# Kernel optimization log

Hardware: AMD Instinct MI355X
Metric: run time of the kernel (lower is better)

## Reference

```python
import jax, jax.numpy as jnp
import numpy as np

NUM_CLASSES = 1000
FEAT_DIM = 256
BATCH = 8192
MARGIN = 5.0
ALPHA = 1.0
BETA = 1.0


def setup_inputs() -> dict:
    key = jax.random.key(0)
    k1, k2, k3 = jax.random.split(key, 3)
    x = jax.random.normal(k1, (BATCH, FEAT_DIM), dtype=jnp.float32)
    labels = jax.random.randint(k2, (BATCH,), 0, NUM_CLASSES, dtype=jnp.int64)
    centers = jax.random.normal(k3, (NUM_CLASSES, FEAT_DIM), dtype=jnp.float32)
    return {"x": x, "labels": labels, "centers": centers}


def reference(x, labels, centers):
    # --- intra-class part ---
    # distmat_intra[i, j] = ||x_i||^2 + ||x_j||^2 - 2 x_i . x_j  (then relu + sqrt)
    mag = jnp.sum(x * x, axis=1)                      # (B,)
    sim = x @ x.T                                     # (B, B)
    d2 = mag[None, :] + mag[:, None] - 2.0 * sim      # (B, B)
    d = jnp.sqrt(jax.nn.relu(d2))                     # (B, B)

    # mask[i, j] = labels[i] == labels[j]; original gathers masked values per row,
    # clamps to [1e-12, 1e12], sorts descending and uses only the top-2 values.
    mask = labels[:, None] == labels[None, :]         # (B, B) bool
    vals = jnp.where(mask, jnp.clip(d, 1e-12, 1e12), -jnp.inf)
    top2, _ = jax.lax.top_k(vals.reshape(-1), 2)      # two largest intra-class dists
    k = 2.0
    loss_intra = k / (1.0 / top2[0] + 1.0 / top2[1])  # harmonic mean * k

    # --- inter-class part (faithful to original broadcasting) ---
    # distmat_inter[i, j] = 2 ||c_j||^2 - 2 c_i . c_j
    cmag = 2.0 * jnp.sum(centers * centers, axis=1)   # (C,)
    inter = cmag[None, :] - 2.0 * (centers @ centers.T)
    inter = jnp.clip(inter.reshape(-1), 1e-12, 1e12)
    loss_inter = jnp.clip(MARGIN - jnp.min(inter), 0.0, 1e6)

    return ALPHA * loss_intra + BETA * loss_inter
```

## Files before the change

### kernel.cpp

```cpp
#include <hip/hip_runtime.h>
#include <math.h>

#define BATCH 8192
#define FEAT  256
#define NCLS  1000

#define NGEMM   528
#define NINTRA  NCLS
#define ROWCAP  24
#define MEMCAP  96


__global__ __launch_bounds__(512) void k_intra(const float* __restrict__ x,
                                               const int* __restrict__ labels,
                                               float* __restrict__ ws) {
    __shared__ __align__(16) float rowS[ROWCAP][256];
    __shared__ int   mem[MEMCAP];
    __shared__ float magS[MEMCAP];
    __shared__ float wred[8];
    __shared__ int cnt;
    int t = threadIdx.x;
    int lane = t & 63, w = t >> 6;
    int c = blockIdx.x;

    if (t == 0) cnt = 0;
    __syncthreads();
    const int4* gl4 = reinterpret_cast<const int4*>(labels);
    #pragma unroll
    for (int k = 0; k < 4; ++k) {
        int idx = t + (k << 9);
        int4 lv = gl4[idx];
        int base = idx << 2;
        if (lv.x == c) { int p = atomicAdd(&cnt, 1); if (p < MEMCAP) mem[p] = base;     }
        if (lv.y == c) { int p = atomicAdd(&cnt, 1); if (p < MEMCAP) mem[p] = base + 1; }
        if (lv.z == c) { int p = atomicAdd(&cnt, 1); if (p < MEMCAP) mem[p] = base + 2; }
        if (lv.w == c) { int p = atomicAdd(&cnt, 1); if (p < MEMCAP) mem[p] = base + 3; }
    }
    __syncthreads();
    int n = cnt < MEMCAP ? cnt : MEMCAP;
    float vmax = 0.0f;
    if (n >= 2) {
        const float4* x4 = reinterpret_cast<const float4*>(x);
        for (int m = w; m < n; m += 8) {
            float4 v = x4[(size_t)mem[m] * 64 + lane];
            if (m < ROWCAP)
                *reinterpret_cast<float4*>(&rowS[m][lane << 2]) = v;
            float s = v.x * v.x + v.y * v.y + v.z * v.z + v.w * v.w;
            #pragma unroll
            for (int o = 32; o > 0; o >>= 1) s += __shfl_xor(s, o);
            if (lane == 0) magS[m] = s;
        }
        __syncthreads();
        int npairs = n * (n - 1) / 2;
        for (int p = w; p < npairs; p += 16) {
            int p2 = p + 8;
            bool has2 = (p2 < npairs);
            int a1 = 0, r1 = p;
            while (r1 >= n - 1 - a1) { r1 -= n - 1 - a1; ++a1; }
            int b1 = a1 + 1 + r1;
            int a2 = a1, b2 = b1;
            if (has2) {
                int r2 = p2; a2 = 0;
                while (r2 >= n - 1 - a2) { r2 -= n - 1 - a2; ++a2; }
                b2 = a2 + 1 + r2;
            }
            float4 va1 = (a1 < ROWCAP) ? *reinterpret_cast<float4*>(&rowS[a1][lane << 2])
                                       : x4[(size_t)mem[a1] * 64 + lane];
            float4 vb1 = (b1 < ROWCAP) ? *reinterpret_cast<float4*>(&rowS[b1][lane << 2])
                                       : x4[(size_t)mem[b1] * 64 + lane];
            float4 va2 = (a2 < ROWCAP) ? *reinterpret_cast<float4*>(&rowS[a2][lane << 2])
                                       : x4[(size_t)mem[a2] * 64 + lane];
            float4 vb2 = (b2 < ROWCAP) ? *reinterpret_cast<float4*>(&rowS[b2][lane << 2])
                                       : x4[(size_t)mem[b2] * 64 + lane];
            float s1 = va1.x * vb1.x + va1.y * vb1.y + va1.z * vb1.z + va1.w * vb1.w;
            float s2 = va2.x * vb2.x + va2.y * vb2.y + va2.z * vb2.z + va2.w * vb2.w;
            #pragma unroll
            for (int o = 32; o > 0; o >>= 1) {
                s1 += __shfl_xor(s1, o);
                s2 += __shfl_xor(s2, o);
            }
            float d2a = magS[a1] + magS[b1] - 2.0f * s1;
            float da  = sqrtf(fmaxf(d2a, 0.0f));
            da = fminf(fmaxf(da, 1e-12f), 1e12f);
            vmax = fmaxf(vmax, da);
            if (has2) {
                float d2b = magS[a2] + magS[b2] - 2.0f * s2;
                float db  = sqrtf(fmaxf(d2b, 0.0f));
                db = fminf(fmaxf(db, 1e-12f), 1e12f);
                vmax = fmaxf(vmax, db);
            }
        }
    }
    if (lane == 0) wred[w] = vmax;
    __syncthreads();
    if (t == 0) {
        float m = 0.0f;
        #pragma unroll
        for (int q = 0; q < 8; ++q) m = fmaxf(m, wred[q]);
        ws[NGEMM + c] = m;
    }
}

__global__ __launch_bounds__(256) void k_inter(const float* __restrict__ centers,
                                               float* __restrict__ ws) {
    __shared__ float As[32][34];
    __shared__ float Bs[32][34];
    __shared__ float cmagI[32], cmagJ[32];
    __shared__ float wred[4];
    int t = threadIdx.x;
    int lane = t & 63, w = t >> 6;

    int bi = 0, rem = blockIdx.x;
    while (rem >= 32 - bi) { rem -= 32 - bi; ++bi; }
    int bj = bi + rem;
    int i0 = bi * 32, j0 = bj * 32;

    for (int q = w; q < 32; q += 4) {
        int gi = i0 + q, gj = j0 + q;
        float sI = 0.0f, sJ = 0.0f;
        if (gi < NCLS) {
            float4 v = reinterpret_cast<const float4*>(centers + (size_t)gi * FEAT)[lane];
            sI = v.x * v.x + v.y * v.y + v.z * v.z + v.w * v.w;
        }
        if (gj < NCLS) {
            float4 v = reinterpret_cast<const float4*>(centers + (size_t)gj * FEAT)[lane];
            sJ = v.x * v.x + v.y * v.y + v.z * v.z + v.w * v.w;
        }
        #pragma unroll
        for (int o = 32; o > 0; o >>= 1) {
            sI += __shfl_xor(sI, o);
            sJ += __shfl_xor(sJ, o);
        }
        if (lane == 0) { cmagI[q] = 2.0f * sI; cmagJ[q] = 2.0f * sJ; }
    }

    int tx = t & 15, ty = t >> 4;
    float acc[2][2] = {{0.f, 0.f}, {0.f, 0.f}};
    for (int kk = 0; kk < FEAT; kk += 32) {
        {
            int row = t >> 3, q = t & 7;
            int col = kk + q * 4;
            int gi = i0 + row, gj = j0 + row;
            float4 av = (gi < NCLS)
                ? *reinterpret_cast<const float4*>(centers + (size_t)gi * FEAT + col)
                : make_float4(0.f, 0.f, 0.f, 0.f);
            float4 bv = (gj < NCLS)
                ? *reinterpret_cast<const float4*>(centers + (size_t)gj * FEAT + col)
                : make_float4(0.f, 0.f, 0.f, 0.f);
            As[q * 4 + 0][row] = av.x; As[q * 4 + 1][row] = av.y;
            As[q * 4 + 2][row] = av.z; As[q * 4 + 3][row] = av.w;
            Bs[q * 4 + 0][row] = bv.x; Bs[q * 4 + 1][row] = bv.y;
            Bs[q * 4 + 2][row] = bv.z; Bs[q * 4 + 3][row] = bv.w;
        }
        __syncthreads();
        #pragma unroll
        for (int k = 0; k < 32; ++k) {
            float2 a2 = *reinterpret_cast<float2*>(&As[k][ty * 2]);
            float2 b2 = *reinterpret_cast<float2*>(&Bs[k][tx * 2]);
            acc[0][0] += a2.x * b2.x; acc[0][1] += a2.x * b2.y;
            acc[1][0] += a2.y * b2.x; acc[1][1] += a2.y * b2.y;
        }
        __syncthreads();
    }
    float lmin = 1e30f;
    #pragma unroll
    for (int jj = 0; jj < 2; ++jj) {
        int J = j0 + tx * 2 + jj;
        #pragma unroll
        for (int ii = 0; ii < 2; ++ii) {
            int I = i0 + ty * 2 + ii;
            if (I < NCLS && J < NCLS) {
                float v1 = cmagJ[tx * 2 + jj] - 2.0f * acc[ii][jj];
                v1 = fminf(fmaxf(v1, 1e-12f), 1e12f);
                float v2 = cmagI[ty * 2 + ii] - 2.0f * acc[ii][jj];
                v2 = fminf(fmaxf(v2, 1e-12f), 1e12f);
                lmin = fminf(lmin, fminf(v1, v2));
            }
        }
    }
    #pragma unroll
    for (int o = 32; o > 0; o >>= 1) lmin = fminf(lmin, __shfl_xor(lmin, o));
    if (lane == 0) wred[w] = lmin;
    __syncthreads();
    if (t == 0) {
        float m = fminf(fminf(wred[0], wred[1]), fminf(wred[2], wred[3]));
        ws[blockIdx.x] = m;
    }
}

__global__ __launch_bounds__(256) void k_final(const float* __restrict__ ws,
                                               float* __restrict__ out) {
    __shared__ float smx[4], smn[4];
    int t = threadIdx.x, lane = t & 63, w = t >> 6;
    float mn = 1e30f, mx = 0.0f;
    for (int i = t; i < NGEMM; i += 256)  mn = fminf(mn, ws[i]);
    for (int i = t; i < NINTRA; i += 256) mx = fmaxf(mx, ws[NGEMM + i]);
    #pragma unroll
    for (int o = 32; o > 0; o >>= 1) {
        mx = fmaxf(mx, __shfl_xor(mx, o));
        mn = fminf(mn, __shfl_xor(mn, o));
    }
    if (lane == 0) { smx[w] = mx; smn[w] = mn; }
    __syncthreads();
    if (t == 0) {
        mx = fmaxf(fmaxf(smx[0], smx[1]), fmaxf(smx[2], smx[3]));
        mn = fminf(fminf(smn[0], smn[1]), fminf(smn[2], smn[3]));
        float M = fmaxf(mx, 1e-12f);
        float r = 1.0f / M;
        float li2 = 2.0f / (r + r);
        float m = fminf(mn, 1e12f);
        float linter = fminf(fmaxf(5.0f - m, 0.0f), 1e6f);
        out[0] = li2 + linter;
    }
}

extern "C" void kernel_launch(void* const* d_in, const int* in_sizes, int n_in,
                              void* d_out, int out_size, void* d_ws, size_t ws_size,
                              hipStream_t stream) {
    const float* x       = (const float*)d_in[0];
    const int*   labels  = (const int*)d_in[1];
    const float* centers = (const float*)d_in[2];
    float*        ws     = (float*)d_ws;
    float*        out    = (float*)d_out;

    k_intra<<<NINTRA, 512, 0, stream>>>(x, labels, ws);
    k_inter<<<NGEMM, 256, 0, stream>>>(centers, ws);
    k_final<<<1, 256, 0, stream>>>(ws, out);
}
```

Measured before the change: 100.4 us.

## Bucket samples by label globally and fuse intra/inter passes into one launch

Each of the 1000 intra blocks used to scan all 8192 labels itself. A prep kernel now computes row norms and buckets sample indices per class with global atomics, after a memset of the counts. The intra pair work is split across 4 blocks per class and merged with the inter-center GEMM blocks into a single launch, which improves occupancy and overlap. In exchange it adds a memset and an extra launch, drops the shared-memory row cache in favour of global (L2) loads, and lowers the per-class member cap to 64.

```diff
diff --git a/kernel.cpp b/kernel.cpp
--- a/kernel.cpp
+++ b/kernel.cpp
@@ -5,104 +5,38 @@
 #define FEAT  256
 #define NCLS  1000
 
-#define NGEMM   528
-#define NINTRA  NCLS
-#define ROWCAP  24
-#define MEMCAP  96
-
-
-__global__ __launch_bounds__(512) void k_intra(const float* __restrict__ x,
-                                               const int* __restrict__ labels,
-                                               float* __restrict__ ws) {
-    __shared__ __align__(16) float rowS[ROWCAP][256];
-    __shared__ int   mem[MEMCAP];
-    __shared__ float magS[MEMCAP];
-    __shared__ float wred[8];
-    __shared__ int cnt;
-    int t = threadIdx.x;
-    int lane = t & 63, w = t >> 6;
-    int c = blockIdx.x;
-
-    if (t == 0) cnt = 0;
-    __syncthreads();
-    const int4* gl4 = reinterpret_cast<const int4*>(labels);
+#define NGEMM  528
+#define REPL   4
+#define NPAIRB (REPL*NCLS)
+#define NBLK   (NGEMM + NPAIRB)
+#define SLOTC  64
+
+
+__global__ __launch_bounds__(256) void k_prep(const float* __restrict__ x,
+                                              const int* __restrict__ labels,
+                                              int* __restrict__ counts,
+                                              int* __restrict__ mem,
+                                              float* __restrict__ mag) {
+    int gw   = (blockIdx.x * 256 + threadIdx.x) >> 6;
+    int lane = threadIdx.x & 63;
+    float4 v = reinterpret_cast<const float4*>(x)[(size_t)gw * 64 + lane];
+    float s = v.x * v.x + v.y * v.y + v.z * v.z + v.w * v.w;
     #pragma unroll
-    for (int k = 0; k < 4; ++k) {
-        int idx = t + (k << 9);
-        int4 lv = gl4[idx];
-        int base = idx << 2;
-        if (lv.x == c) { int p = atomicAdd(&cnt, 1); if (p < MEMCAP) mem[p] = base;     }
-        if (lv.y == c) { int p = atomicAdd(&cnt, 1); if (p < MEMCAP) mem[p] = base + 1; }
-        if (lv.z == c) { int p = atomicAdd(&cnt, 1); if (p < MEMCAP) mem[p] = base + 2; }
-        if (lv.w == c) { int p = atomicAdd(&cnt, 1); if (p < MEMCAP) mem[p] = base + 3; }
-    }
-    __syncthreads();
-    int n = cnt < MEMCAP ? cnt : MEMCAP;
-    float vmax = 0.0f;
-    if (n >= 2) {
-        const float4* x4 = reinterpret_cast<const float4*>(x);
-        for (int m = w; m < n; m += 8) {
-            float4 v = x4[(size_t)mem[m] * 64 + lane];
-            if (m < ROWCAP)
-                *reinterpret_cast<float4*>(&rowS[m][lane << 2]) = v;
-            float s = v.x * v.x + v.y * v.y + v.z * v.z + v.w * v.w;
-            #pragma unroll
-            for (int o = 32; o > 0; o >>= 1) s += __shfl_xor(s, o);
-            if (lane == 0) magS[m] = s;
-        }
-        __syncthreads();
-        int npairs = n * (n - 1) / 2;
-        for (int p = w; p < npairs; p += 16) {
-            int p2 = p + 8;
-            bool has2 = (p2 < npairs);
-            int a1 = 0, r1 = p;
-            while (r1 >= n - 1 - a1) { r1 -= n - 1 - a1; ++a1; }
-            int b1 = a1 + 1 + r1;
-            int a2 = a1, b2 = b1;
-            if (has2) {
-                int r2 = p2; a2 = 0;
-                while (r2 >= n - 1 - a2) { r2 -= n - 1 - a2; ++a2; }
-                b2 = a2 + 1 + r2;
-            }
-            float4 va1 = (a1 < ROWCAP) ? *reinterpret_cast<float4*>(&rowS[a1][lane << 2])
-                                       : x4[(size_t)mem[a1] * 64 + lane];
-            float4 vb1 = (b1 < ROWCAP) ? *reinterpret_cast<float4*>(&rowS[b1][lane << 2])
-                                       : x4[(size_t)mem[b1] * 64 + lane];
-            float4 va2 = (a2 < ROWCAP) ? *reinterpret_cast<float4*>(&rowS[a2][lane << 2])
-                                       : x4[(size_t)mem[a2] * 64 + lane];
-            float4 vb2 = (b2 < ROWCAP) ? *reinterpret_cast<float4*>(&rowS[b2][lane << 2])
-                                       : x4[(size_t)mem[b2] * 64 + lane];
-            float s1 = va1.x * vb1.x + va1.y * vb1.y + va1.z * vb1.z + va1.w * vb1.w;
-            float s2 = va2.x * vb2.x + va2.y * vb2.y + va2.z * vb2.z + va2.w * vb2.w;
-            #pragma unroll
-            for (int o = 32; o > 0; o >>= 1) {
-                s1 += __shfl_xor(s1, o);
-                s2 += __shfl_xor(s2, o);
-            }
-            float d2a = magS[a1] + magS[b1] - 2.0f * s1;
-            float da  = sqrtf(fmaxf(d2a, 0.0f));
-            da = fminf(fmaxf(da, 1e-12f), 1e12f);
-            vmax = fmaxf(vmax, da);
-            if (has2) {
-                float d2b = magS[a2] + magS[b2] - 2.0f * s2;
-                float db  = sqrtf(fmaxf(d2b, 0.0f));
-                db = fminf(fmaxf(db, 1e-12f), 1e12f);
-                vmax = fmaxf(vmax, db);
-            }
-        }
-    }
-    if (lane == 0) wred[w] = vmax;
-    __syncthreads();
-    if (t == 0) {
-        float m = 0.0f;
-        #pragma unroll
-        for (int q = 0; q < 8; ++q) m = fmaxf(m, wred[q]);
-        ws[NGEMM + c] = m;
-    }
-}
-
-__global__ __launch_bounds__(256) void k_inter(const float* __restrict__ centers,
-                                               float* __restrict__ ws) {
+    for (int o = 32; o > 0; o >>= 1) s += __shfl_xor(s, o);
+    if (lane == 0) {
+        mag[gw] = s;
+        int c = labels[gw];
+        int pos = atomicAdd(&counts[c], 1);
+        if (pos < SLOTC) mem[c * SLOTC + pos] = gw;
+    }
+}
+
+__global__ __launch_bounds__(256) void k_fused(const float* __restrict__ x,
+                                               const float* __restrict__ centers,
+                                               const int* __restrict__ counts,
+                                               const int* __restrict__ mem,
+                                               const float* __restrict__ mag,
+                                               float* __restrict__ part) {
     __shared__ float As[32][34];
     __shared__ float Bs[32][34];
     __shared__ float cmagI[32], cmagJ[32];
@@ -110,91 +44,145 @@
     int t = threadIdx.x;
     int lane = t & 63, w = t >> 6;
 
-    int bi = 0, rem = blockIdx.x;
-    while (rem >= 32 - bi) { rem -= 32 - bi; ++bi; }
-    int bj = bi + rem;
-    int i0 = bi * 32, j0 = bj * 32;
-
-    for (int q = w; q < 32; q += 4) {
-        int gi = i0 + q, gj = j0 + q;
-        float sI = 0.0f, sJ = 0.0f;
-        if (gi < NCLS) {
-            float4 v = reinterpret_cast<const float4*>(centers + (size_t)gi * FEAT)[lane];
-            sI = v.x * v.x + v.y * v.y + v.z * v.z + v.w * v.w;
-        }
-        if (gj < NCLS) {
-            float4 v = reinterpret_cast<const float4*>(centers + (size_t)gj * FEAT)[lane];
-            sJ = v.x * v.x + v.y * v.y + v.z * v.z + v.w * v.w;
-        }
+    if (blockIdx.x < NGEMM) {
+        int bi = 0, rem = blockIdx.x;
+        while (rem >= 32 - bi) { rem -= 32 - bi; ++bi; }
+        int bj = bi + rem;
+        int i0 = bi * 32, j0 = bj * 32;
+
+        for (int q = w; q < 32; q += 4) {
+            int gi = i0 + q, gj = j0 + q;
+            float sI = 0.0f, sJ = 0.0f;
+            if (gi < NCLS) {
+                float4 v = reinterpret_cast<const float4*>(centers + (size_t)gi * FEAT)[lane];
+                sI = v.x * v.x + v.y * v.y + v.z * v.z + v.w * v.w;
+            }
+            if (gj < NCLS) {
+                float4 v = reinterpret_cast<const float4*>(centers + (size_t)gj * FEAT)[lane];
+                sJ = v.x * v.x + v.y * v.y + v.z * v.z + v.w * v.w;
+            }
+            #pragma unroll
+            for (int o = 32; o > 0; o >>= 1) {
+                sI += __shfl_xor(sI, o);
+                sJ += __shfl_xor(sJ, o);
+            }
+            if (lane == 0) { cmagI[q] = 2.0f * sI; cmagJ[q] = 2.0f * sJ; }
+        }
+
+        int tx = t & 15, ty = t >> 4;
+        float acc[2][2] = {{0.f, 0.f}, {0.f, 0.f}};
+        for (int kk = 0; kk < FEAT; kk += 32) {
+            {
+                int row = t >> 3, q = t & 7;
+                int col = kk + q * 4;
+                int gi = i0 + row, gj = j0 + row;
+                float4 av = (gi < NCLS)
+                    ? *reinterpret_cast<const float4*>(centers + (size_t)gi * FEAT + col)
+                    : make_float4(0.f, 0.f, 0.f, 0.f);
+                float4 bv = (gj < NCLS)
+                    ? *reinterpret_cast<const float4*>(centers + (size_t)gj * FEAT + col)
+                    : make_float4(0.f, 0.f, 0.f, 0.f);
+                As[q * 4 + 0][row] = av.x; As[q * 4 + 1][row] = av.y;
+                As[q * 4 + 2][row] = av.z; As[q * 4 + 3][row] = av.w;
+                Bs[q * 4 + 0][row] = bv.x; Bs[q * 4 + 1][row] = bv.y;
+                Bs[q * 4 + 2][row] = bv.z; Bs[q * 4 + 3][row] = bv.w;
+            }
+            __syncthreads();
+            #pragma unroll
+            for (int k = 0; k < 32; ++k) {
+                float2 a2 = *reinterpret_cast<float2*>(&As[k][ty * 2]);
+                float2 b2 = *reinterpret_cast<float2*>(&Bs[k][tx * 2]);
+                acc[0][0] += a2.x * b2.x; acc[0][1] += a2.x * b2.y;
+                acc[1][0] += a2.y * b2.x; acc[1][1] += a2.y * b2.y;
+            }
+            __syncthreads();
+        }
+        float lmin = 1e30f;
         #pragma unroll
-        for (int o = 32; o > 0; o >>= 1) {
-            sI += __shfl_xor(sI, o);
-            sJ += __shfl_xor(sJ, o);
-        }
-        if (lane == 0) { cmagI[q] = 2.0f * sI; cmagJ[q] = 2.0f * sJ; }
-    }
-
-    int tx = t & 15, ty = t >> 4;
-    float acc[2][2] = {{0.f, 0.f}, {0.f, 0.f}};
-    for (int kk = 0; kk < FEAT; kk += 32) {
-        {
-            int row = t >> 3, q = t & 7;
-            int col = kk + q * 4;
-            int gi = i0 + row, gj = j0 + row;
-            float4 av = (gi < NCLS)
-                ? *reinterpret_cast<const float4*>(centers + (size_t)gi * FEAT + col)
-                : make_float4(0.f, 0.f, 0.f, 0.f);
-            float4 bv = (gj < NCLS)
-                ? *reinterpret_cast<const float4*>(centers + (size_t)gj * FEAT + col)
-                : make_float4(0.f, 0.f, 0.f, 0.f);
-            As[q * 4 + 0][row] = av.x; As[q * 4 + 1][row] = av.y;
-            As[q * 4 + 2][row] = av.z; As[q * 4 + 3][row] = av.w;
-            Bs[q * 4 + 0][row] = bv.x; Bs[q * 4 + 1][row] = bv.y;
-            Bs[q * 4 + 2][row] = bv.z; Bs[q * 4 + 3][row] = bv.w;
-        }
+        for (int jj = 0; jj < 2; ++jj) {
+            int J = j0 + tx * 2 + jj;
+            #pragma unroll
+            for (int ii = 0; ii < 2; ++ii) {
+                int I = i0 + ty * 2 + ii;
+                if (I < NCLS && J < NCLS) {
+                    float v1 = cmagJ[tx * 2 + jj] - 2.0f * acc[ii][jj];
+                    v1 = fminf(fmaxf(v1, 1e-12f), 1e12f);
+                    float v2 = cmagI[ty * 2 + ii] - 2.0f * acc[ii][jj];
+                    v2 = fminf(fmaxf(v2, 1e-12f), 1e12f);
+                    lmin = fminf(lmin, fminf(v1, v2));
+                }
+            }
+        }
+        #pragma unroll
+        for (int o = 32; o > 0; o >>= 1) lmin = fminf(lmin, __shfl_xor(lmin, o));
+        if (lane == 0) wred[w] = lmin;
         __syncthreads();
-        #pragma unroll
-        for (int k = 0; k < 32; ++k) {
-            float2 a2 = *reinterpret_cast<float2*>(&As[k][ty * 2]);
-            float2 b2 = *reinterpret_cast<float2*>(&Bs[k][tx * 2]);
-            acc[0][0] += a2.x * b2.x; acc[0][1] += a2.x * b2.y;
-            acc[1][0] += a2.y * b2.x; acc[1][1] += a2.y * b2.y;
-        }
+        if (t == 0) {
+            float m = fminf(fminf(wred[0], wred[1]), fminf(wred[2], wred[3]));
+            part[blockIdx.x] = m;
+        }
+    } else {
+        int bidp = blockIdx.x - NGEMM;
+        int c = bidp >> 2, r = bidp & 3;
+        int n = counts[c]; if (n > SLOTC) n = SLOTC;
+        float vmax = 0.0f;
+        if (n >= 2) {
+            const float4* x4 = reinterpret_cast<const float4*>(x);
+            const int* memc = mem + c * SLOTC;
+            int npairs = n * (n - 1) / 2;
+            for (int p = r * 4 + w; p < npairs; p += 32) {
+                int p2 = p + 16;
+                bool has2 = (p2 < npairs);
+                int a1 = 0, r1 = p;
+                while (r1 >= n - 1 - a1) { r1 -= n - 1 - a1; ++a1; }
+                int b1 = a1 + 1 + r1;
+                int a2 = a1, b2 = b1;
+                if (has2) {
+                    int r2 = p2; a2 = 0;
+                    while (r2 >= n - 1 - a2) { r2 -= n - 1 - a2; ++a2; }
+                    b2 = a2 + 1 + r2;
+                }
+                int ia1 = memc[a1], ib1 = memc[b1];
+                int ia2 = memc[a2], ib2 = memc[b2];
+                float4 va1 = x4[(size_t)ia1 * 64 + lane];
+                float4 vb1 = x4[(size_t)ib1 * 64 + lane];
+                float4 va2 = x4[(size_t)ia2 * 64 + lane];
+                float4 vb2 = x4[(size_t)ib2 * 64 + lane];
+                float s1 = va1.x * vb1.x + va1.y * vb1.y + va1.z * vb1.z + va1.w * vb1.w;
+                float s2 = va2.x * vb2.x + va2.y * vb2.y + va2.z * vb2.z + va2.w * vb2.w;
+                #pragma unroll
+                for (int o = 32; o > 0; o >>= 1) {
+                    s1 += __shfl_xor(s1, o);
+                    s2 += __shfl_xor(s2, o);
+                }
+                float d2a = mag[ia1] + mag[ib1] - 2.0f * s1;
+                float da  = sqrtf(fmaxf(d2a, 0.0f));
+                da = fminf(fmaxf(da, 1e-12f), 1e12f);
+                vmax = fmaxf(vmax, da);
+                if (has2) {
+                    float d2b = mag[ia2] + mag[ib2] - 2.0f * s2;
+                    float db  = sqrtf(fmaxf(d2b, 0.0f));
+                    db = fminf(fmaxf(db, 1e-12f), 1e12f);
+                    vmax = fmaxf(vmax, db);
+                }
+            }
+        }
+        if (lane == 0) wred[w] = vmax;
         __syncthreads();
-    }
-    float lmin = 1e30f;
-    #pragma unroll
-    for (int jj = 0; jj < 2; ++jj) {
-        int J = j0 + tx * 2 + jj;
-        #pragma unroll
-        for (int ii = 0; ii < 2; ++ii) {
-            int I = i0 + ty * 2 + ii;
-            if (I < NCLS && J < NCLS) {
-                float v1 = cmagJ[tx * 2 + jj] - 2.0f * acc[ii][jj];
-                v1 = fminf(fmaxf(v1, 1e-12f), 1e12f);
-                float v2 = cmagI[ty * 2 + ii] - 2.0f * acc[ii][jj];
-                v2 = fminf(fmaxf(v2, 1e-12f), 1e12f);
-                lmin = fminf(lmin, fminf(v1, v2));
-            }
-        }
-    }
-    #pragma unroll
-    for (int o = 32; o > 0; o >>= 1) lmin = fminf(lmin, __shfl_xor(lmin, o));
-    if (lane == 0) wred[w] = lmin;
-    __syncthreads();
-    if (t == 0) {
-        float m = fminf(fminf(wred[0], wred[1]), fminf(wred[2], wred[3]));
-        ws[blockIdx.x] = m;
-    }
-}
-
-__global__ __launch_bounds__(256) void k_final(const float* __restrict__ ws,
+        if (t == 0) {
+            float m = fmaxf(fmaxf(wred[0], wred[1]), fmaxf(wred[2], wred[3]));
+            part[blockIdx.x] = m;
+        }
+    }
+}
+
+__global__ __launch_bounds__(256) void k_final(const float* __restrict__ part,
                                                float* __restrict__ out) {
     __shared__ float smx[4], smn[4];
     int t = threadIdx.x, lane = t & 63, w = t >> 6;
     float mn = 1e30f, mx = 0.0f;
-    for (int i = t; i < NGEMM; i += 256)  mn = fminf(mn, ws[i]);
-    for (int i = t; i < NINTRA; i += 256) mx = fmaxf(mx, ws[NGEMM + i]);
+    for (int i = t; i < NGEMM; i += 256)  mn = fminf(mn, part[i]);
+    for (int i = t; i < NPAIRB; i += 256) mx = fmaxf(mx, part[NGEMM + i]);
     #pragma unroll
     for (int o = 32; o > 0; o >>= 1) {
         mx = fmaxf(mx, __shfl_xor(mx, o));
@@ -220,10 +208,15 @@
     const float* x       = (const float*)d_in[0];
     const int*   labels  = (const int*)d_in[1];
     const float* centers = (const float*)d_in[2];
-    float*        ws     = (float*)d_ws;
-    float*        out    = (float*)d_out;
-
-    k_intra<<<NINTRA, 512, 0, stream>>>(x, labels, ws);
-    k_inter<<<NGEMM, 256, 0, stream>>>(centers, ws);
-    k_final<<<1, 256, 0, stream>>>(ws, out);
-}
+    char* wsb = (char*)d_ws;
+    int*   counts = (int*)(wsb);
+    int*   mem    = (int*)(wsb + 4096);
+    float* mag    = (float*)(wsb + 262144);
+    float* part   = (float*)(wsb + 294912);
+    float* out    = (float*)d_out;
+
+    hipMemsetAsync(counts, 0, NCLS * sizeof(int), stream);
+    k_prep<<<BATCH / 4, 256, 0, stream>>>(x, labels, counts, mem, mag);
+    k_fused<<<NBLK, 256, 0, stream>>>(x, centers, counts, mem, mag, part);
+    k_final<<<1, 256, 0, stream>>>(part, out);
+}
```

After: 92.77 us. 1.08x faster.
